# Kernel optimization log

Hardware: AMD Instinct MI355X
Metric: run time of the kernel (lower is better)

The kernel has to match this reference:

```python
import jax, jax.numpy as jnp
import numpy as np

P, N, B, F, H, O, D, A = 3, 6144, 3072, 512, 8, 32, 256, 128
HI = F // H  # per-head input dim = 64


def setup_inputs() -> dict:
    key = jax.random.key(0)
    ks = jax.random.split(key, 12)
    s = 0.05
    return dict(
        features=jax.random.normal(ks[0], (P, N, F), jnp.float32),
        biases=jax.random.normal(ks[1], (P, N, N), jnp.float32),
        batch_nodes=jax.random.randint(ks[2], (P, B), 0, N),
        RL_thresholds=jax.random.uniform(ks[3], (P, 1), jnp.float32),
        Wc1=jax.random.normal(ks[4], (P, H, O, HI), jnp.float32) * s,
        bc1=jnp.zeros((P, H, O), jnp.float32),
        a1=jax.random.normal(ks[5], (P, H, O), jnp.float32) * s,
        ab1=jnp.zeros((P, H), jnp.float32),
        a2=jax.random.normal(ks[6], (P, H, O), jnp.float32) * s,
        ab2=jnp.zeros((P, H), jnp.float32),
        Wm=jax.random.normal(ks[7], (D, D), jnp.float32) * s,
        bm=jnp.zeros((D,), jnp.float32),
        w_omega=jax.random.normal(ks[8], (D, A), jnp.float32) * s,
        b_omega=jnp.zeros((A,), jnp.float32),
        u_omega=jax.random.normal(ks[9], (A,), jnp.float32) * s,
    )


def reference(features, biases, batch_nodes, RL_thresholds, Wc1, bc1, a1, ab1,
              a2, ab2, Wm, bm, w_omega, b_omega, u_omega):
    embeds = []
    for i in range(P):  # fixed small relation loop (bias_mx_len)
        idx = batch_nodes[i]
        bf = features[i][idx]                      # [B, F]
        bb = biases[i][idx][:, idx]                # [B, B] bias mask
        xh = bf.reshape(B, H, HI).transpose(1, 0, 2)   # [H, B, HI] per-head feature slices
        # Attn_Head: conv1d(k=1) == per-head linear projection
        seq = jnp.einsum('hbi,hoi->hbo', xh, Wc1[i]) + bc1[i][:, None, :]  # [H, B, O]
        f1 = jnp.einsum('hbo,ho->hb', seq, a1[i]) + ab1[i][:, None]       # [H, B]
        f2 = jnp.einsum('hbo,ho->hb', seq, a2[i]) + ab2[i][:, None]       # [H, B]
        logits = jax.nn.leaky_relu(f1[:, :, None] + f2[:, None, :], 0.01)  # [H, B, B]
        coefs = jax.nn.softmax(logits + bb[None], axis=-1)                 # [H, B, B]
        out = jax.nn.elu(jnp.einsum('hqk,hko->hqo', coefs, seq))           # [H, B, O]
        h1 = out.transpose(1, 0, 2).reshape(B, H * O)                      # concat heads -> [B, D]
        embeds.append(h1 @ Wm.T + bm)                                      # w_multi
    multi = jnp.stack(embeds, axis=1)              # [B, P, D]
    inputs = multi * RL_thresholds[None]           # RL scaling, [P,1] broadcasts
    # SimpleAttnLayer: semantic attention over relations
    v = jnp.tanh(jnp.einsum('bpd,da->bpa', inputs, w_omega) + b_omega)
    vu = jnp.einsum('bpa,a->bp', v, u_omega)
    alphas = jax.nn.softmax(vu, axis=-1)           # [B, P]
    return jnp.sum(inputs * alphas[:, :, None], axis=1)  # [B, D]
```

## Files before the change

kernel.cpp:

```cpp
#include <hip/hip_runtime.h>
#include <cstdint>
#include <cstddef>

#define PP 3
#define NN 6144
#define BB 3072
#define FF 512
#define HH 8
#define OO 32
#define DD 256
#define AA 128
#define M0 10.0f
#define LOG2E 1.44269504088896340736f
#define KSPLIT 4
#define KRANGE (BB/KSPLIT)
#define NT (KRANGE/32)

typedef __attribute__((ext_vector_type(8))) short short8;
typedef __attribute__((ext_vector_type(4))) float f32x4;

__device__ __forceinline__ unsigned short f2bf(float x){
  union { float f; unsigned u; } v; v.f = x;
  unsigned r = v.u + 0x7fffu + ((v.u >> 16) & 1u);
  return (unsigned short)(r >> 16);
}

__device__ __forceinline__ float fexp2(float x){
#if __has_builtin(__builtin_amdgcn_exp2f)
  return __builtin_amdgcn_exp2f(x);
#else
  return exp2f(x);
#endif
}

__device__ __forceinline__ f32x4 mfma16(short8 a, short8 b, f32x4 c){
  return __builtin_amdgcn_mfma_f32_16x16x32_bf16(a, b, c, 0, 0, 0);
}

__global__ __launch_bounds__(256) void k_seq(
    const float* __restrict__ features, const int* __restrict__ batch_nodes,
    const float* __restrict__ Wc1, const float* __restrict__ bc1,
    const float* __restrict__ a1, const float* __restrict__ ab1,
    const float* __restrict__ a2, const float* __restrict__ ab2,
    unsigned short* __restrict__ seqT, float* __restrict__ f1g, float* __restrict__ f2g)
{
  int i = blockIdx.z, h = blockIdx.y, b0 = blockIdx.x * 8;
  int t = threadIdx.x;
  __shared__ float xs[8][64];
  __shared__ float wt[64][33];
  __shared__ float a1s[32], a2s[32], bcs[32];
  __shared__ float sst[32][9];
  const float* W = Wc1 + (size_t)(i*HH + h) * OO * 64;
  for (int e = t; e < 2048; e += 256){ int o = e >> 6, c = e & 63; wt[c][o] = W[e]; }
  if (t < 32){
    a1s[t] = a1[(i*HH+h)*OO + t];
    a2s[t] = a2[(i*HH+h)*OO + t];
    bcs[t] = bc1[(i*HH+h)*OO + t];
  }
  for (int e = t; e < 512; e += 256){
    int bl = e >> 6, c = e & 63;
    int row = batch_nodes[i*BB + b0 + bl];
    xs[bl][c] = features[((size_t)i*NN + row)*FF + h*64 + c];
  }
  __syncthreads();
  int bl = t >> 5, o = t & 31;
  float acc = bcs[o];
  #pragma unroll
  for (int c = 0; c < 64; c++) acc += xs[bl][c] * wt[c][o];
  float v1 = acc * a1s[o], v2 = acc * a2s[o];
  #pragma unroll
  for (int s = 16; s >= 1; s >>= 1){ v1 += __shfl_xor(v1, s); v2 += __shfl_xor(v2, s); }
  if (o == 0){
    f1g[(i*HH+h)*BB + b0 + bl] = (v1 + ab1[i*HH+h]) * LOG2E;
    f2g[(i*HH+h)*BB + b0 + bl] = (v2 + ab2[i*HH+h]) * LOG2E;
  }
  sst[o][bl] = acc;
  __syncthreads();
  {
    int o2 = t >> 3, b2 = t & 7;
    seqT[((size_t)(i*HH+h)*OO + o2)*BB + b0 + b2] = f2bf(sst[o2][b2]);
  }
}

__global__ __launch_bounds__(256) void k_gather(
    const float* __restrict__ biases, const int* __restrict__ batch_nodes,
    float* __restrict__ bbg, int i_base, int nbuf)
{
  int i = i_base + blockIdx.z;
  int q0 = blockIdx.x * 2;
  int t = threadIdx.x;
  __shared__ float rowbuf[2][NN];
  int r0 = batch_nodes[i*BB + q0];
  int r1 = batch_nodes[i*BB + q0 + 1];
  const float4* s0 = (const float4*)(biases + ((size_t)i*NN + r0)*NN);
  const float4* s1 = (const float4*)(biases + ((size_t)i*NN + r1)*NN);
  #pragma unroll
  for (int e = 0; e < NN/4; e += 256){
    ((float4*)rowbuf[0])[e + t] = s0[e + t];
    ((float4*)rowbuf[1])[e + t] = s1[e + t];
  }
  const int* ci = batch_nodes + i*BB;
  float* dst0 = bbg + ((size_t)(i % nbuf)*BB + q0)*BB;
  float* dst1 = dst0 + BB;
  __syncthreads();
  #pragma unroll 4
  for (int c = 0; c < BB; c += 256){
    int k = c + t;
    int col = ci[k];
    dst0[k] = (rowbuf[0][col] - M0) * LOG2E;
    dst1[k] = (rowbuf[1][col] - M0) * LOG2E;
  }
}

__global__ __launch_bounds__(256, 3) void k_attn(
    const float* __restrict__ bbg, const unsigned short* __restrict__ seqT,
    const float* __restrict__ f1g, const float* __restrict__ f2g,
    float* __restrict__ Lp, float* __restrict__ h1p, int i_base, int nbuf)
{
  int i = i_base + blockIdx.z;
  int ks = blockIdx.y;
  int q0 = blockIdx.x * 32;
  int kbase = ks * KRANGE;
  int t = threadIdx.x;
  int w = t >> 6, lane = t & 63;
  int qf = lane & 15, kq = lane >> 4;
  f32x4 acc[2][2][2] = {};
  float Ls[2][2] = {{0.f,0.f},{0.f,0.f}};
  float f1r[2][2];
  #pragma unroll
  for (int hh = 0; hh < 2; hh++)
  #pragma unroll
  for (int qh = 0; qh < 2; qh++){
    int h = w*2 + hh;
    f1r[hh][qh] = f1g[(i*HH+h)*BB + q0 + qh*16 + qf];
  }
  const float* bbb = bbg + (size_t)(i % nbuf)*BB*BB;
  const float* bbp0 = bbb + (size_t)(q0 + qf)*BB + kbase + kq*8;
  const float* bbp1 = bbp0 + (size_t)16*BB;
  const float* f2p0 = f2g + ((size_t)(i*HH + w*2 + 0))*BB + kbase + kq*8;
  const float* f2p1 = f2p0 + BB;
  const unsigned short* sq00 = seqT + ((size_t)(i*HH + w*2 + 0)*OO + qf)*BB + kbase + kq*8;
  const unsigned short* sq01 = sq00 + (size_t)16*BB;
  const unsigned short* sq10 = sq00 + (size_t)OO*BB;
  const unsigned short* sq11 = sq10 + (size_t)16*BB;

  struct Tile {
    f32x4 bb[2][2];
    f32x4 f2[2][2];
    short8 sq[2][2];
  };
  auto loadt = [&](Tile &T, int d){
    #pragma unroll
    for (int c = 0; c < 2; c++){
      T.bb[0][c] = *(const f32x4*)(bbp0 + d + c*4);
      T.bb[1][c] = *(const f32x4*)(bbp1 + d + c*4);
      T.f2[0][c] = *(const f32x4*)(f2p0 + d + c*4);
      T.f2[1][c] = *(const f32x4*)(f2p1 + d + c*4);
    }
    T.sq[0][0] = *(const short8*)(sq00 + d);
    T.sq[0][1] = *(const short8*)(sq01 + d);
    T.sq[1][0] = *(const short8*)(sq10 + d);
    T.sq[1][1] = *(const short8*)(sq11 + d);
  };
  auto compt = [&](const Tile &T){
    #pragma unroll
    for (int hh = 0; hh < 2; hh++){
      short8 af0, af1;
      #pragma unroll
      for (int j = 0; j < 8; j++){
        float f2v = T.f2[hh][j>>2][j&3];
        float s0 = f1r[hh][0] + f2v;
        s0 = fmaxf(s0, 0.01f*s0) + T.bb[0][j>>2][j&3];
        float s1 = f1r[hh][1] + f2v;
        s1 = fmaxf(s1, 0.01f*s1) + T.bb[1][j>>2][j&3];
        float e0 = fexp2(s0);
        float e1 = fexp2(s1);
        Ls[hh][0] += e0; Ls[hh][1] += e1;
        af0[j] = (short)f2bf(e0);
        af1[j] = (short)f2bf(e1);
      }
      acc[hh][0][0] = mfma16(af0, T.sq[hh][0], acc[hh][0][0]);
      acc[hh][0][1] = mfma16(af0, T.sq[hh][1], acc[hh][0][1]);
      acc[hh][1][0] = mfma16(af1, T.sq[hh][0], acc[hh][1][0]);
      acc[hh][1][1] = mfma16(af1, T.sq[hh][1], acc[hh][1][1]);
    }
  };

  Tile ta, tb;
  loadt(ta, 0);
  for (int it = 0; it < NT; it += 2){
    loadt(tb, (it+1)*32);
    compt(ta);
    if (it + 2 < NT) loadt(ta, (it+2)*32);
    compt(tb);
  }

  #pragma unroll
  for (int hh = 0; hh < 2; hh++)
  #pragma unroll
  for (int qh = 0; qh < 2; qh++){
    float v = Ls[hh][qh];
    v += __shfl_xor(v, 16);
    v += __shfl_xor(v, 32);
    if (kq == 0)
      Lp[(((size_t)ks*PP + i)*HH + w*2 + hh)*BB + q0 + qh*16 + qf] = v;
  }
  #pragma unroll
  for (int hh = 0; hh < 2; hh++){
    int h = w*2 + hh;
    #pragma unroll
    for (int qh = 0; qh < 2; qh++)
    #pragma unroll
    for (int oh = 0; oh < 2; oh++)
    #pragma unroll
    for (int r = 0; r < 4; r++){
      int q = q0 + qh*16 + kq*4 + r;
      int o = qf + oh*16;
      h1p[(((size_t)ks*PP + i)*BB + q)*DD + h*OO + o] = acc[hh][qh][oh][r];
    }
  }
}

__global__ __launch_bounds__(256) void k_twm(const float* __restrict__ Wm, float* __restrict__ wmT){
  int e = blockIdx.x, d = threadIdx.x;
  wmT[(size_t)e*DD + d] = Wm[(size_t)d*DD + e];
}

__global__ __launch_bounds__(256) void k_final(
    const float* __restrict__ h1p, const float* __restrict__ Lp,
    const float* __restrict__ wmT, const float* __restrict__ bm,
    const float* __restrict__ RL, const float* __restrict__ w_omega, const float* __restrict__ b_omega,
    const float* __restrict__ u_omega, float* __restrict__ out)
{
  __shared__ float buf[48*256];
  __shared__ float wred[4][24];
  __shared__ float alph[3][16];
  __shared__ float linvs[48][8];
  const size_t PB = (size_t)PP*BB*DD;
  const size_t KL = (size_t)PP*HH*BB;
  int t = threadIdx.x;
  int lane = t & 63, w = t >> 6;
  int b0 = blockIdx.x * 16;
  for (int e = t; e < 48*8; e += 256){
    int pb = e >> 3, h = e & 7;
    int p = pb / 16, bl = pb & 15;
    size_t off = ((size_t)p*HH + h)*BB + b0 + bl;
    float L = Lp[off] + Lp[off+KL] + Lp[off+2*KL] + Lp[off+3*KL];
    linvs[pb][h] = 1.f / L;
  }
  __syncthreads();
  for (int e = t; e < 48*256; e += 256){
    int pb = e >> 8, d = e & 255;
    int p = pb / 16, bl = pb & 15;
    size_t off = ((size_t)p*BB + b0 + bl)*DD + d;
    float v = h1p[off] + h1p[off + PB] + h1p[off + 2*PB] + h1p[off + 3*PB];
    v *= linvs[pb][d >> 5];
    buf[e] = (v > 0.f) ? v : (__expf(v) - 1.f);
  }
  __syncthreads();
  float acc[48];
  #pragma unroll
  for (int x = 0; x < 48; x++) acc[x] = 0.f;
  for (int e = 0; e < 256; e += 4){
    float w0 = wmT[(e+0)*DD + t];
    float w1 = wmT[(e+1)*DD + t];
    float w2 = wmT[(e+2)*DD + t];
    float w3 = wmT[(e+3)*DD + t];
    #pragma unroll
    for (int pb = 0; pb < 48; pb++){
      float4 hv = *(const float4*)&buf[pb*256 + e];
      acc[pb] += hv.x*w0 + hv.y*w1 + hv.z*w2 + hv.w*w3;
    }
  }
  __syncthreads();
  {
    float bmv = bm[t];
    #pragma unroll
    for (int p = 0; p < 3; p++){
      float rl = RL[p];
      #pragma unroll
      for (int bl = 0; bl < 16; bl++)
        buf[(p*16+bl)*256 + t] = (acc[p*16+bl] + bmv) * rl;
    }
  }
  __syncthreads();
  int a = t & 127, g = t >> 7;
  float acc2[24];
  #pragma unroll
  for (int x = 0; x < 24; x++) acc2[x] = 0.f;
  for (int e = 0; e < 256; e += 4){
    float w0 = w_omega[(e+0)*AA + a];
    float w1 = w_omega[(e+1)*AA + a];
    float w2 = w_omega[(e+2)*AA + a];
    float w3 = w_omega[(e+3)*AA + a];
    #pragma unroll
    for (int p = 0; p < 3; p++){
      #pragma unroll
      for (int bl = 0; bl < 8; bl++){
        float4 iv = *(const float4*)&buf[(p*16 + g*8 + bl)*256 + e];
        acc2[p*8+bl] += iv.x*w0 + iv.y*w1 + iv.z*w2 + iv.w*w3;
      }
    }
  }
  {
    float bo = b_omega[a], uo = u_omega[a];
    #pragma unroll
    for (int x = 0; x < 24; x++){
      float v = tanhf(acc2[x] + bo) * uo;
      #pragma unroll
      for (int s = 32; s >= 1; s >>= 1) v += __shfl_xor(v, s);
      if (lane == 0) wred[w][x] = v;
    }
  }
  __syncthreads();
  if (t < 16){
    int b = t;
    int g2 = b >> 3, bl2 = b & 7;
    float vu[3];
    #pragma unroll
    for (int p = 0; p < 3; p++){
      int j = p*8 + bl2;
      vu[p] = wred[g2*2 + 0][j] + wred[g2*2 + 1][j];
    }
    float mx = fmaxf(vu[0], fmaxf(vu[1], vu[2]));
    float e0 = __expf(vu[0]-mx), e1 = __expf(vu[1]-mx), e2 = __expf(vu[2]-mx);
    float inv = 1.f / (e0+e1+e2);
    alph[0][b] = e0*inv; alph[1][b] = e1*inv; alph[2][b] = e2*inv;
  }
  __syncthreads();
  #pragma unroll
  for (int bl = 0; bl < 16; bl++){
    float o = buf[(0*16+bl)*256 + t]*alph[0][bl]
            + buf[(1*16+bl)*256 + t]*alph[1][bl]
            + buf[(2*16+bl)*256 + t]*alph[2][bl];
    out[(size_t)(b0+bl)*DD + t] = o;
  }
}

extern "C" void kernel_launch(void* const* d_in, const int* in_sizes, int n_in,
                              void* d_out, int out_size, void* d_ws, size_t ws_size,
                              hipStream_t stream)
{
  const float* features = (const float*)d_in[0];
  const float* biases   = (const float*)d_in[1];
  const int*   batch_nodes = (const int*)d_in[2];
  const float* RL   = (const float*)d_in[3];
  const float* Wc1  = (const float*)d_in[4];
  const float* bc1  = (const float*)d_in[5];
  const float* a1   = (const float*)d_in[6];
  const float* ab1  = (const float*)d_in[7];
  const float* a2   = (const float*)d_in[8];
  const float* ab2  = (const float*)d_in[9];
  const float* Wm   = (const float*)d_in[10];
  const float* bm   = (const float*)d_in[11];
  const float* w_omega = (const float*)d_in[12];
  const float* b_omega = (const float*)d_in[13];
  const float* u_omega = (const float*)d_in[14];
  float* out = (float*)d_out;

  size_t sz_bbg1 = (size_t)BB*BB*4;
  size_t sz_seqT = (size_t)PP*HH*OO*BB*2;
  size_t sz_f    = (size_t)PP*HH*BB*4;
  size_t sz_h1   = (size_t)PP*BB*DD*4;
  size_t sz_wmT  = (size_t)DD*DD*4;
  size_t sz_Lp   = (size_t)KSPLIT*PP*HH*BB*4;
  size_t fixed = sz_seqT + 2*sz_f + (size_t)KSPLIT*sz_h1 + sz_wmT + sz_Lp + 16*256;
  int nbuf = (ws_size >= fixed + 3*sz_bbg1 + 256) ? 3 : 1;

  char* p = (char*)d_ws;
  auto take = [&](size_t bytes)->char*{ char* r = p; p += (bytes + 255) & ~(size_t)255; return r; };
  float* bbg  = (float*)take(sz_bbg1 * (size_t)nbuf);
  unsigned short* seqT = (unsigned short*)take(sz_seqT);
  float* f1g  = (float*)take(sz_f);
  float* f2g  = (float*)take(sz_f);
  float* Lp   = (float*)take(sz_Lp);
  float* h1p  = (float*)take(sz_h1 * (size_t)KSPLIT);
  float* wmT  = (float*)take(sz_wmT);

  k_twm<<<dim3(DD), dim3(DD), 0, stream>>>(Wm, wmT);
  k_seq<<<dim3(BB/8, HH, PP), dim3(256), 0, stream>>>(features, batch_nodes, Wc1, bc1, a1, ab1, a2, ab2, seqT, f1g, f2g);
  int nloop = (nbuf == 3) ? 1 : 3;
  int z = (nbuf == 3) ? 3 : 1;
  for (int r = 0; r < nloop; r++){
    k_gather<<<dim3(BB/2, 1, z), dim3(256), 0, stream>>>(biases, batch_nodes, bbg, r, nbuf);
    k_attn<<<dim3(BB/32, KSPLIT, z), dim3(256), 0, stream>>>(bbg, seqT, f1g, f2g, Lp, h1p, r, nbuf);
  }
  k_final<<<dim3(BB/16), dim3(256), 0, stream>>>(h1p, Lp, wmT, bm, RL, w_omega, b_omega, u_omega, out);
}
```

Baseline: 961.8 us.

## Split attention heads across two blocks to cut registers and raise occupancy

```diff
diff --git a/kernel.cpp b/kernel.cpp
--- a/kernel.cpp
+++ b/kernel.cpp
@@ -112,78 +112,67 @@
   }
 }
 
-__global__ __launch_bounds__(256, 3) void k_attn(
+__global__ __launch_bounds__(256, 4) void k_attn(
     const float* __restrict__ bbg, const unsigned short* __restrict__ seqT,
     const float* __restrict__ f1g, const float* __restrict__ f2g,
     float* __restrict__ Lp, float* __restrict__ h1p, int i_base, int nbuf)
 {
   int i = i_base + blockIdx.z;
-  int ks = blockIdx.y;
+  int yy = blockIdx.y;
+  int ks = yy >> 1, hg = yy & 1;
   int q0 = blockIdx.x * 32;
   int kbase = ks * KRANGE;
   int t = threadIdx.x;
   int w = t >> 6, lane = t & 63;
+  int h = hg*4 + w;
   int qf = lane & 15, kq = lane >> 4;
-  f32x4 acc[2][2][2] = {};
-  float Ls[2][2] = {{0.f,0.f},{0.f,0.f}};
-  float f1r[2][2];
-  #pragma unroll
-  for (int hh = 0; hh < 2; hh++)
-  #pragma unroll
-  for (int qh = 0; qh < 2; qh++){
-    int h = w*2 + hh;
-    f1r[hh][qh] = f1g[(i*HH+h)*BB + q0 + qh*16 + qf];
-  }
+  f32x4 acc[2][2] = {};
+  float Ls[2] = {0.f, 0.f};
+  float f1r[2];
+  #pragma unroll
+  for (int qh = 0; qh < 2; qh++)
+    f1r[qh] = f1g[(i*HH+h)*BB + q0 + qh*16 + qf];
   const float* bbb = bbg + (size_t)(i % nbuf)*BB*BB;
   const float* bbp0 = bbb + (size_t)(q0 + qf)*BB + kbase + kq*8;
   const float* bbp1 = bbp0 + (size_t)16*BB;
-  const float* f2p0 = f2g + ((size_t)(i*HH + w*2 + 0))*BB + kbase + kq*8;
-  const float* f2p1 = f2p0 + BB;
-  const unsigned short* sq00 = seqT + ((size_t)(i*HH + w*2 + 0)*OO + qf)*BB + kbase + kq*8;
-  const unsigned short* sq01 = sq00 + (size_t)16*BB;
-  const unsigned short* sq10 = sq00 + (size_t)OO*BB;
-  const unsigned short* sq11 = sq10 + (size_t)16*BB;
+  const float* f2p  = f2g + ((size_t)(i*HH + h))*BB + kbase + kq*8;
+  const unsigned short* sq0 = seqT + ((size_t)(i*HH + h)*OO + qf)*BB + kbase + kq*8;
+  const unsigned short* sq1 = sq0 + (size_t)16*BB;
 
   struct Tile {
     f32x4 bb[2][2];
-    f32x4 f2[2][2];
-    short8 sq[2][2];
+    f32x4 f2[2];
+    short8 sq[2];
   };
   auto loadt = [&](Tile &T, int d){
     #pragma unroll
     for (int c = 0; c < 2; c++){
       T.bb[0][c] = *(const f32x4*)(bbp0 + d + c*4);
       T.bb[1][c] = *(const f32x4*)(bbp1 + d + c*4);
-      T.f2[0][c] = *(const f32x4*)(f2p0 + d + c*4);
-      T.f2[1][c] = *(const f32x4*)(f2p1 + d + c*4);
-    }
-    T.sq[0][0] = *(const short8*)(sq00 + d);
-    T.sq[0][1] = *(const short8*)(sq01 + d);
-    T.sq[1][0] = *(const short8*)(sq10 + d);
-    T.sq[1][1] = *(const short8*)(sq11 + d);
+      T.f2[c]    = *(const f32x4*)(f2p  + d + c*4);
+    }
+    T.sq[0] = *(const short8*)(sq0 + d);
+    T.sq[1] = *(const short8*)(sq1 + d);
   };
   auto compt = [&](const Tile &T){
-    #pragma unroll
-    for (int hh = 0; hh < 2; hh++){
-      short8 af0, af1;
-      #pragma unroll
-      for (int j = 0; j < 8; j++){
-        float f2v = T.f2[hh][j>>2][j&3];
-        float s0 = f1r[hh][0] + f2v;
-        s0 = fmaxf(s0, 0.01f*s0) + T.bb[0][j>>2][j&3];
-        float s1 = f1r[hh][1] + f2v;
-        s1 = fmaxf(s1, 0.01f*s1) + T.bb[1][j>>2][j&3];
-        float e0 = fexp2(s0);
-        float e1 = fexp2(s1);
-        Ls[hh][0] += e0; Ls[hh][1] += e1;
-        af0[j] = (short)f2bf(e0);
-        af1[j] = (short)f2bf(e1);
-      }
-      acc[hh][0][0] = mfma16(af0, T.sq[hh][0], acc[hh][0][0]);
-      acc[hh][0][1] = mfma16(af0, T.sq[hh][1], acc[hh][0][1]);
-      acc[hh][1][0] = mfma16(af1, T.sq[hh][0], acc[hh][1][0]);
-      acc[hh][1][1] = mfma16(af1, T.sq[hh][1], acc[hh][1][1]);
-    }
+    short8 af0, af1;
+    #pragma unroll
+    for (int j = 0; j < 8; j++){
+      float f2v = T.f2[j>>2][j&3];
+      float s0 = f1r[0] + f2v;
+      s0 = fmaxf(s0, 0.01f*s0) + T.bb[0][j>>2][j&3];
+      float s1 = f1r[1] + f2v;
+      s1 = fmaxf(s1, 0.01f*s1) + T.bb[1][j>>2][j&3];
+      float e0 = fexp2(s0);
+      float e1 = fexp2(s1);
+      Ls[0] += e0; Ls[1] += e1;
+      af0[j] = (short)f2bf(e0);
+      af1[j] = (short)f2bf(e1);
+    }
+    acc[0][0] = mfma16(af0, T.sq[0], acc[0][0]);
+    acc[0][1] = mfma16(af0, T.sq[1], acc[0][1]);
+    acc[1][0] = mfma16(af1, T.sq[0], acc[1][0]);
+    acc[1][1] = mfma16(af1, T.sq[1], acc[1][1]);
   };
 
   Tile ta, tb;
@@ -196,28 +185,22 @@
   }
 
   #pragma unroll
-  for (int hh = 0; hh < 2; hh++)
-  #pragma unroll
   for (int qh = 0; qh < 2; qh++){
-    float v = Ls[hh][qh];
+    float v = Ls[qh];
     v += __shfl_xor(v, 16);
     v += __shfl_xor(v, 32);
     if (kq == 0)
-      Lp[(((size_t)ks*PP + i)*HH + w*2 + hh)*BB + q0 + qh*16 + qf] = v;
-  }
-  #pragma unroll
-  for (int hh = 0; hh < 2; hh++){
-    int h = w*2 + hh;
-    #pragma unroll
-    for (int qh = 0; qh < 2; qh++)
-    #pragma unroll
-    for (int oh = 0; oh < 2; oh++)
-    #pragma unroll
-    for (int r = 0; r < 4; r++){
-      int q = q0 + qh*16 + kq*4 + r;
-      int o = qf + oh*16;
-      h1p[(((size_t)ks*PP + i)*BB + q)*DD + h*OO + o] = acc[hh][qh][oh][r];
-    }
+      Lp[(((size_t)ks*PP + i)*HH + h)*BB + q0 + qh*16 + qf] = v;
+  }
+  #pragma unroll
+  for (int qh = 0; qh < 2; qh++)
+  #pragma unroll
+  for (int oh = 0; oh < 2; oh++)
+  #pragma unroll
+  for (int r = 0; r < 4; r++){
+    int q = q0 + qh*16 + kq*4 + r;
+    int o = qf + oh*16;
+    h1p[(((size_t)ks*PP + i)*BB + q)*DD + h*OO + o] = acc[qh][oh][r];
   }
 }
 
@@ -383,7 +366,7 @@
   int z = (nbuf == 3) ? 3 : 1;
   for (int r = 0; r < nloop; r++){
     k_gather<<<dim3(BB/2, 1, z), dim3(256), 0, stream>>>(biases, batch_nodes, bbg, r, nbuf);
-    k_attn<<<dim3(BB/32, KSPLIT, z), dim3(256), 0, stream>>>(bbg, seqT, f1g, f2g, Lp, h1p, r, nbuf);
+    k_attn<<<dim3(BB/32, KSPLIT*2, z), dim3(256), 0, stream>>>(bbg, seqT, f1g, f2g, Lp, h1p, r, nbuf);
   }
   k_final<<<dim3(BB/16), dim3(256), 0, stream>>>(h1p, Lp, wmT, bm, RL, w_omega, b_omega, u_omega, out);
 }
```

After: 953.6 us. Within noise of the previous version (-0.9%).
